# Kernel optimization log

Measured on AMD Instinct MI355X. Metric: run time of the kernel, lower is better.

The kernel has to match this reference:

```python
import jax, jax.numpy as jnp
import numpy as np

B, TV, TH, F, H, D = 16, 128, 64, 512, 512, 256


def setup_inputs() -> dict:
    key = jax.random.key(0)
    ks = jax.random.split(key, 6)
    return {
        "v": jax.random.normal(ks[0], (B, TV, F), dtype=jnp.float32),
        "h": jax.random.normal(ks[1], (B, TH, H), dtype=jnp.float32),
        "W": jax.random.normal(ks[2], (F, D), dtype=jnp.float32) * 0.05,
        "U": jax.random.normal(ks[3], (H, D), dtype=jnp.float32) * 0.05,
        "b": jax.random.normal(ks[4], (D,), dtype=jnp.float32) * 0.05,
        "w": jax.random.normal(ks[5], (D, 1), dtype=jnp.float32) * 0.05,
    }


def reference(v, h, W, U, b, w):
    # v: [B, Tv, F] video features; h: [B, Th, H] decoder hidden states
    Wv = jnp.einsum("btf,fd->btd", v, W)      # [B, Tv, D]
    Uh = jnp.einsum("bsh,hd->bsd", h, U)      # [B, Th, D]
    # Broadcast add -> [B, Th, Tv, D], tanh nonlinearity (additive attention)
    f = jnp.tanh(Uh[:, :, None, :] + Wv[:, None, :, :] + b)
    q = jnp.einsum("bstd,d->bst", f, w[:, 0])  # scores [B, Th, Tv]
    beta = jax.nn.softmax(q, axis=-1)           # softmax over Tv (axis -2 of q[..., None])
    u = jnp.einsum("bst,btf->bsf", beta, v)    # context [B, Th, F]
    return u
```

## Files before the change

kernel.cpp:

```cpp
#include <hip/hip_runtime.h>
#include <hip/hip_bf16.h>

#define BB 16
#define TV 128
#define TH 64
#define FF 512
#define HH 512
#define DD 256

#define LOG2E2 2.8853900817779268f

typedef __attribute__((ext_vector_type(8))) short bf16x8;
typedef __attribute__((ext_vector_type(4))) float f32x4;

__device__ __forceinline__ float fast_exp2(float x) {
#if __has_builtin(__builtin_amdgcn_exp2f)
  return __builtin_amdgcn_exp2f(x);
#else
  return __expf(x * 0.6931471805599453f);
#endif
}
__device__ __forceinline__ float fast_rcp(float x) {
#if __has_builtin(__builtin_amdgcn_rcpf)
  return __builtin_amdgcn_rcpf(x);
#else
  return 1.0f / x;
#endif
}
__device__ __forceinline__ unsigned short f2bf(float x) {
  union { float f; unsigned u; } a; a.f = x;
  unsigned r = a.u + 0x7fffu + ((a.u >> 16) & 1u);
  return (unsigned short)(r >> 16);
}
__device__ __forceinline__ float bf2f(unsigned short x) {
  union { unsigned u; float f; } a; a.u = ((unsigned)x) << 16;
  return a.f;
}

#define NT_V 262144
#define NT_H 131072
#define NT_W 32768
__global__ __launch_bounds__(256) void convert_kernel(
    const float* __restrict__ v, const float* __restrict__ h,
    const float* __restrict__ W, const float* __restrict__ U,
    unsigned short* __restrict__ vb, unsigned short* __restrict__ hb,
    unsigned short* __restrict__ WT, unsigned short* __restrict__ UT) {
  int task = blockIdx.x * 256 + threadIdx.x;
  if (task < NT_V) {
    float4 x = ((const float4*)v)[task];
    ushort4 o = make_ushort4(f2bf(x.x), f2bf(x.y), f2bf(x.z), f2bf(x.w));
    *(ushort4*)&vb[(size_t)task * 4] = o;
  } else if (task < NT_V + NT_H) {
    int t2 = task - NT_V;
    float4 x = ((const float4*)h)[t2];
    ushort4 o = make_ushort4(f2bf(x.x), f2bf(x.y), f2bf(x.z), f2bf(x.w));
    *(ushort4*)&hb[(size_t)t2 * 4] = o;
  } else {
    int t2 = task - NT_V - NT_H;
    const float* S;
    unsigned short* Dt;
    if (t2 < NT_W) { S = W; Dt = WT; } else { S = U; Dt = UT; t2 -= NT_W; }
    int n = t2 & 255, k4 = t2 >> 8;
    float a0 = S[(k4 * 4 + 0) * 256 + n];
    float a1 = S[(k4 * 4 + 1) * 256 + n];
    float a2 = S[(k4 * 4 + 2) * 256 + n];
    float a3 = S[(k4 * 4 + 3) * 256 + n];
    ushort4 o = make_ushort4(f2bf(a0), f2bf(a1), f2bf(a2), f2bf(a3));
    *(ushort4*)&Dt[(size_t)n * 512 + k4 * 4] = o;
  }
}

__global__ __launch_bounds__(256) void mfma_gemm_kernel(
    const unsigned short* __restrict__ Av, const unsigned short* __restrict__ Ah,
    const unsigned short* __restrict__ WT, const unsigned short* __restrict__ UT,
    const float* __restrict__ bias, float* __restrict__ Wv2T,
    float* __restrict__ Uh2) {
  const int bid = blockIdx.x;
  const unsigned short* A;
  const unsigned short* BT;
  int mt, nt;
  bool is_wv;
  if (bid < 128) {
    A = Av; BT = WT; is_wv = true;
    mt = bid >> 3; nt = bid & 7;
  } else {
    const int b2 = bid - 128;
    A = Ah; BT = UT; is_wv = false;
    mt = b2 >> 3; nt = b2 & 7;
  }
  const int wv   = threadIdx.x >> 6;
  const int lane = threadIdx.x & 63;
  const int m0   = mt * 128 + wv * 32;
  const int n0   = nt * 32;
  const int r16  = lane & 15;
  const int quad = lane >> 4;

  const unsigned short* a0p = A + (size_t)(m0 + r16) * 512 + quad * 8;
  const unsigned short* a1p = a0p + 16 * 512;
  const unsigned short* b0p = BT + (size_t)(n0 + r16) * 512 + quad * 8;
  const unsigned short* b1p = b0p + 16 * 512;

  f32x4 acc00 = {0.f, 0.f, 0.f, 0.f};
  f32x4 acc01 = {0.f, 0.f, 0.f, 0.f};
  f32x4 acc10 = {0.f, 0.f, 0.f, 0.f};
  f32x4 acc11 = {0.f, 0.f, 0.f, 0.f};

#pragma unroll 4
  for (int kc = 0; kc < 16; kc++) {
    bf16x8 a0 = *(const bf16x8*)(a0p + kc * 32);
    bf16x8 a1 = *(const bf16x8*)(a1p + kc * 32);
    bf16x8 b0 = *(const bf16x8*)(b0p + kc * 32);
    bf16x8 b1 = *(const bf16x8*)(b1p + kc * 32);
    acc00 = __builtin_amdgcn_mfma_f32_16x16x32_bf16(a0, b0, acc00, 0, 0, 0);
    acc01 = __builtin_amdgcn_mfma_f32_16x16x32_bf16(a0, b1, acc01, 0, 0, 0);
    acc10 = __builtin_amdgcn_mfma_f32_16x16x32_bf16(a1, b0, acc10, 0, 0, 0);
    acc11 = __builtin_amdgcn_mfma_f32_16x16x32_bf16(a1, b1, acc11, 0, 0, 0);
  }

  if (is_wv) {
    const int tb = (m0 & 127) + quad * 4;
    float* Wb = Wv2T + (size_t)mt * 32768;
    float4 s00, s01, s10, s11;
#pragma unroll
    for (int r = 0; r < 4; r++) {
      (&s00.x)[r] = acc00[r] * LOG2E2;
      (&s01.x)[r] = acc01[r] * LOG2E2;
      (&s10.x)[r] = acc10[r] * LOG2E2;
      (&s11.x)[r] = acc11[r] * LOG2E2;
    }
    *(float4*)&Wb[(size_t)(n0 + r16) * 128 + tb]           = s00;
    *(float4*)&Wb[(size_t)(n0 + r16) * 128 + tb + 16]      = s10;
    *(float4*)&Wb[(size_t)(n0 + 16 + r16) * 128 + tb]      = s01;
    *(float4*)&Wb[(size_t)(n0 + 16 + r16) * 128 + tb + 16] = s11;
  } else {
    const float bj0 = bias[n0 + r16];
    const float bj1 = bias[n0 + 16 + r16];
#pragma unroll
    for (int r = 0; r < 4; r++) {
      const int row0 = m0 + quad * 4 + r;
      Uh2[(size_t)row0 * 256 + n0 + r16]             = (acc00[r] + bj0) * LOG2E2;
      Uh2[(size_t)row0 * 256 + n0 + 16 + r16]        = (acc01[r] + bj1) * LOG2E2;
      Uh2[(size_t)(row0 + 16) * 256 + n0 + r16]      = (acc10[r] + bj0) * LOG2E2;
      Uh2[(size_t)(row0 + 16) * 256 + n0 + 16 + r16] = (acc11[r] + bj1) * LOG2E2;
    }
  }
}

__global__ __launch_bounds__(512) void attn_fused_kernel(
    const float* __restrict__ Wv2T, const float* __restrict__ Uh2,
    const float* __restrict__ wg, const unsigned short* __restrict__ vb16,
    float* __restrict__ u) {
  __shared__ float UhS[2 * 256];
  __shared__ float wS[256];
  __shared__ float pS[8 * 2 * 128];
  __shared__ float bS[2 * 128];
  __shared__ float mW[4];
  __shared__ float sW[4];

  const int tid = threadIdx.x;
  const int b   = blockIdx.x >> 5;
  const int sg  = blockIdx.x & 31;
  const int s0  = sg * 2;

  if (tid < 128) {
    const int row = tid >> 6, q4 = (tid & 63) << 2;
    *(float4*)&UhS[row * 256 + q4] =
        *(const float4*)&Uh2[(size_t)(b * 64 + s0 + row) * 256 + q4];
  } else if (tid < 192) {
    const int q4 = (tid - 128) << 2;
    *(float4*)&wS[q4] = *(const float4*)&wg[q4];
  }
  __syncthreads();

  {
    const int t4 = tid & 31;
    const int dg = (tid >> 5) & 7;
    const int s  = tid >> 8;
    const float* wvb = Wv2T + (size_t)b * 32768 + (size_t)dg * 32 * 128 + t4 * 4;
    const float4* uhq = (const float4*)&UhS[s * 256 + dg * 32];
    const float4* wq  = (const float4*)&wS[dg * 32];
    float4 acc = {0.f, 0.f, 0.f, 0.f};
#pragma unroll
    for (int jq = 0; jq < 8; jq++) {
      float4 uh4 = uhq[jq];
      float4 w4  = wq[jq];
#pragma unroll
      for (int jj = 0; jj < 4; jj++) {
        float4 a  = *(const float4*)(wvb + (jq * 4 + jj) * 128);
        float uh = (&uh4.x)[jj];
        float ww = (&w4.x)[jj];
        acc.x = fmaf(ww, fast_rcp(fast_exp2(a.x + uh) + 1.0f), acc.x);
        acc.y = fmaf(ww, fast_rcp(fast_exp2(a.y + uh) + 1.0f), acc.y);
        acc.z = fmaf(ww, fast_rcp(fast_exp2(a.z + uh) + 1.0f), acc.z);
        acc.w = fmaf(ww, fast_rcp(fast_exp2(a.w + uh) + 1.0f), acc.w);
      }
    }
    *(float4*)&pS[(dg * 2 + s) * 128 + t4 * 4] = acc;
  }
  __syncthreads();

  float qv = 0.0f, ev = 0.0f;
  const int wvid = tid >> 6, lane = tid & 63;
  if (tid < 256) {
    const int s_l = tid >> 7, t = tid & 127;
    float ssum = 0.0f;
#pragma unroll
    for (int dg = 0; dg < 8; dg++) ssum += pS[(dg * 2 + s_l) * 128 + t];
    qv = ssum * (-LOG2E2);
    float m = qv;
#pragma unroll
    for (int off = 32; off > 0; off >>= 1) m = fmaxf(m, __shfl_xor(m, off, 64));
    if (lane == 0) mW[wvid] = m;
  }
  __syncthreads();
  if (tid < 256) {
    float m = fmaxf(mW[wvid], mW[wvid ^ 1]);
    ev = fast_exp2(qv - m);
    float ssum = ev;
#pragma unroll
    for (int off = 32; off > 0; off >>= 1) ssum += __shfl_xor(ssum, off, 64);
    if (lane == 0) sW[wvid] = ssum;
  }
  __syncthreads();
  if (tid < 256) {
    const int s_l = tid >> 7, t = tid & 127;
    bS[s_l * 128 + t] = ev * fast_rcp(sW[wvid] + sW[wvid ^ 1]);
  }
  __syncthreads();

  const unsigned short* vb2 = vb16 + (size_t)b * TV * FF;
  const int f = tid;
  float a0 = 0.f, a1 = 0.f;
#pragma unroll 4
  for (int tg = 0; tg < 128; tg += 4) {
    float4 b0 = *(const float4*)&bS[0 * 128 + tg];
    float4 b1 = *(const float4*)&bS[1 * 128 + tg];
    float v0 = bf2f(vb2[(tg + 0) * 512 + f]);
    float v1 = bf2f(vb2[(tg + 1) * 512 + f]);
    float v2 = bf2f(vb2[(tg + 2) * 512 + f]);
    float v3 = bf2f(vb2[(tg + 3) * 512 + f]);
    a0 = fmaf(b0.x, v0, a0); a0 = fmaf(b0.y, v1, a0);
    a0 = fmaf(b0.z, v2, a0); a0 = fmaf(b0.w, v3, a0);
    a1 = fmaf(b1.x, v0, a1); a1 = fmaf(b1.y, v1, a1);
    a1 = fmaf(b1.z, v2, a1); a1 = fmaf(b1.w, v3, a1);
  }
  float* urow = u + (size_t)(b * 64 + s0) * 512;
  urow[0 * 512 + f] = a0;
  urow[1 * 512 + f] = a1;
}

extern "C" void kernel_launch(void* const* d_in, const int* in_sizes, int n_in,
                              void* d_out, int out_size, void* d_ws, size_t ws_size,
                              hipStream_t stream) {
  const float* v  = (const float*)d_in[0];
  const float* h  = (const float*)d_in[1];
  const float* W  = (const float*)d_in[2];
  const float* U  = (const float*)d_in[3];
  const float* bb = (const float*)d_in[4];
  const float* w  = (const float*)d_in[5];
  float* u = (float*)d_out;

  float* Wv2T = (float*)d_ws;
  float* Uh2  = Wv2T + (size_t)2048 * 256;
  unsigned short* vb16 = (unsigned short*)(Uh2 + (size_t)1024 * 256);
  unsigned short* hb16 = vb16 + (size_t)2048 * 512;
  unsigned short* WT   = hb16 + (size_t)1024 * 512;
  unsigned short* UT   = WT + (size_t)256 * 512;

  convert_kernel<<<1792, 256, 0, stream>>>(v, h, W, U, vb16, hb16, WT, UT);
  mfma_gemm_kernel<<<192, 256, 0, stream>>>(vb16, hb16, WT, UT, bb, Wv2T, Uh2);
  attn_fused_kernel<<<512, 512, 0, stream>>>(Wv2T, Uh2, w, vb16, u);
}
```

Measured before the change: 97.97 us.

## Fuse bf16 conversion into GEMM, stage transposed weights in LDS, drop convert kernel

Removes the separate conversion kernel. The GEMM now loads fp32 activations directly and packs them to bf16 in registers. Each block transposes its W/U slice into padded LDS as bf16. The attention context pass reads fp32 v directly instead of the bf16 copy. This saves one launch and the extra write/read round trip through the workspace. In exchange, each GEMM block redundantly converts its weight slice, and the A loads and the final v reads move twice as many bytes.

New measurement: 98.93 us. About the same (+1.0%).

```diff
diff --git a/kernel.cpp b/kernel.cpp
--- a/kernel.cpp
+++ b/kernel.cpp
@@ -32,73 +32,63 @@
   unsigned r = a.u + 0x7fffu + ((a.u >> 16) & 1u);
   return (unsigned short)(r >> 16);
 }
-__device__ __forceinline__ float bf2f(unsigned short x) {
-  union { unsigned u; float f; } a; a.u = ((unsigned)x) << 16;
-  return a.f;
-}
-
-#define NT_V 262144
-#define NT_H 131072
-#define NT_W 32768
-__global__ __launch_bounds__(256) void convert_kernel(
+__device__ __forceinline__ bf16x8 pack_bf8(float4 lo, float4 hi) {
+  bf16x8 r;
+  r[0] = (short)f2bf(lo.x); r[1] = (short)f2bf(lo.y);
+  r[2] = (short)f2bf(lo.z); r[3] = (short)f2bf(lo.w);
+  r[4] = (short)f2bf(hi.x); r[5] = (short)f2bf(hi.y);
+  r[6] = (short)f2bf(hi.z); r[7] = (short)f2bf(hi.w);
+  return r;
+}
+
+#define BT_STRIDE 520
+__global__ __launch_bounds__(256) void mfma_gemm_kernel(
     const float* __restrict__ v, const float* __restrict__ h,
     const float* __restrict__ W, const float* __restrict__ U,
-    unsigned short* __restrict__ vb, unsigned short* __restrict__ hb,
-    unsigned short* __restrict__ WT, unsigned short* __restrict__ UT) {
-  int task = blockIdx.x * 256 + threadIdx.x;
-  if (task < NT_V) {
-    float4 x = ((const float4*)v)[task];
-    ushort4 o = make_ushort4(f2bf(x.x), f2bf(x.y), f2bf(x.z), f2bf(x.w));
-    *(ushort4*)&vb[(size_t)task * 4] = o;
-  } else if (task < NT_V + NT_H) {
-    int t2 = task - NT_V;
-    float4 x = ((const float4*)h)[t2];
-    ushort4 o = make_ushort4(f2bf(x.x), f2bf(x.y), f2bf(x.z), f2bf(x.w));
-    *(ushort4*)&hb[(size_t)t2 * 4] = o;
-  } else {
-    int t2 = task - NT_V - NT_H;
-    const float* S;
-    unsigned short* Dt;
-    if (t2 < NT_W) { S = W; Dt = WT; } else { S = U; Dt = UT; t2 -= NT_W; }
-    int n = t2 & 255, k4 = t2 >> 8;
-    float a0 = S[(k4 * 4 + 0) * 256 + n];
-    float a1 = S[(k4 * 4 + 1) * 256 + n];
-    float a2 = S[(k4 * 4 + 2) * 256 + n];
-    float a3 = S[(k4 * 4 + 3) * 256 + n];
-    ushort4 o = make_ushort4(f2bf(a0), f2bf(a1), f2bf(a2), f2bf(a3));
-    *(ushort4*)&Dt[(size_t)n * 512 + k4 * 4] = o;
-  }
-}
-
-__global__ __launch_bounds__(256) void mfma_gemm_kernel(
-    const unsigned short* __restrict__ Av, const unsigned short* __restrict__ Ah,
-    const unsigned short* __restrict__ WT, const unsigned short* __restrict__ UT,
     const float* __restrict__ bias, float* __restrict__ Wv2T,
     float* __restrict__ Uh2) {
+  __shared__ unsigned short BTs[32 * BT_STRIDE];
+
   const int bid = blockIdx.x;
-  const unsigned short* A;
-  const unsigned short* BT;
+  const float* A;
+  const float* Bsrc;
   int mt, nt;
   bool is_wv;
   if (bid < 128) {
-    A = Av; BT = WT; is_wv = true;
+    A = v; Bsrc = W; is_wv = true;
     mt = bid >> 3; nt = bid & 7;
   } else {
     const int b2 = bid - 128;
-    A = Ah; BT = UT; is_wv = false;
+    A = h; Bsrc = U; is_wv = false;
     mt = b2 >> 3; nt = b2 & 7;
   }
-  const int wv   = threadIdx.x >> 6;
-  const int lane = threadIdx.x & 63;
+  const int tid  = threadIdx.x;
+  const int wv   = tid >> 6;
+  const int lane = tid & 63;
   const int m0   = mt * 128 + wv * 32;
   const int n0   = nt * 32;
   const int r16  = lane & 15;
   const int quad = lane >> 4;
 
-  const unsigned short* a0p = A + (size_t)(m0 + r16) * 512 + quad * 8;
-  const unsigned short* a1p = a0p + 16 * 512;
-  const unsigned short* b0p = BT + (size_t)(n0 + r16) * 512 + quad * 8;
-  const unsigned short* b1p = b0p + 16 * 512;
+  {
+    const int kr = tid >> 3;
+    const int c4 = (tid & 7) << 2;
+#pragma unroll 4
+    for (int p = 0; p < 16; p++) {
+      const int k = p * 32 + kr;
+      float4 wrow = *(const float4*)&Bsrc[(size_t)k * 256 + n0 + c4];
+      BTs[(c4 + 0) * BT_STRIDE + k] = f2bf(wrow.x);
+      BTs[(c4 + 1) * BT_STRIDE + k] = f2bf(wrow.y);
+      BTs[(c4 + 2) * BT_STRIDE + k] = f2bf(wrow.z);
+      BTs[(c4 + 3) * BT_STRIDE + k] = f2bf(wrow.w);
+    }
+  }
+  __syncthreads();
+
+  const float* a0p = A + (size_t)(m0 + r16) * 512 + quad * 8;
+  const float* a1p = a0p + 16 * 512;
+  const unsigned short* bt0 = &BTs[r16 * BT_STRIDE + quad * 8];
+  const unsigned short* bt1 = &BTs[(16 + r16) * BT_STRIDE + quad * 8];
 
   f32x4 acc00 = {0.f, 0.f, 0.f, 0.f};
   f32x4 acc01 = {0.f, 0.f, 0.f, 0.f};
@@ -107,10 +97,14 @@
 
 #pragma unroll 4
   for (int kc = 0; kc < 16; kc++) {
-    bf16x8 a0 = *(const bf16x8*)(a0p + kc * 32);
-    bf16x8 a1 = *(const bf16x8*)(a1p + kc * 32);
-    bf16x8 b0 = *(const bf16x8*)(b0p + kc * 32);
-    bf16x8 b1 = *(const bf16x8*)(b1p + kc * 32);
+    float4 a0lo = *(const float4*)(a0p + kc * 32);
+    float4 a0hi = *(const float4*)(a0p + kc * 32 + 4);
+    float4 a1lo = *(const float4*)(a1p + kc * 32);
+    float4 a1hi = *(const float4*)(a1p + kc * 32 + 4);
+    bf16x8 a0 = pack_bf8(a0lo, a0hi);
+    bf16x8 a1 = pack_bf8(a1lo, a1hi);
+    bf16x8 b0 = *(const bf16x8*)(bt0 + kc * 32);
+    bf16x8 b1 = *(const bf16x8*)(bt1 + kc * 32);
     acc00 = __builtin_amdgcn_mfma_f32_16x16x32_bf16(a0, b0, acc00, 0, 0, 0);
     acc01 = __builtin_amdgcn_mfma_f32_16x16x32_bf16(a0, b1, acc01, 0, 0, 0);
     acc10 = __builtin_amdgcn_mfma_f32_16x16x32_bf16(a1, b0, acc10, 0, 0, 0);
@@ -148,7 +142,7 @@
 
 __global__ __launch_bounds__(512) void attn_fused_kernel(
     const float* __restrict__ Wv2T, const float* __restrict__ Uh2,
-    const float* __restrict__ wg, const unsigned short* __restrict__ vb16,
+    const float* __restrict__ wg, const float* __restrict__ v,
     float* __restrict__ u) {
   __shared__ float UhS[2 * 256];
   __shared__ float wS[256];
@@ -228,17 +222,17 @@
   }
   __syncthreads();
 
-  const unsigned short* vb2 = vb16 + (size_t)b * TV * FF;
+  const float* vb2 = v + (size_t)b * TV * FF;
   const int f = tid;
   float a0 = 0.f, a1 = 0.f;
 #pragma unroll 4
   for (int tg = 0; tg < 128; tg += 4) {
     float4 b0 = *(const float4*)&bS[0 * 128 + tg];
     float4 b1 = *(const float4*)&bS[1 * 128 + tg];
-    float v0 = bf2f(vb2[(tg + 0) * 512 + f]);
-    float v1 = bf2f(vb2[(tg + 1) * 512 + f]);
-    float v2 = bf2f(vb2[(tg + 2) * 512 + f]);
-    float v3 = bf2f(vb2[(tg + 3) * 512 + f]);
+    float v0 = vb2[(tg + 0) * 512 + f];
+    float v1 = vb2[(tg + 1) * 512 + f];
+    float v2 = vb2[(tg + 2) * 512 + f];
+    float v3 = vb2[(tg + 3) * 512 + f];
     a0 = fmaf(b0.x, v0, a0); a0 = fmaf(b0.y, v1, a0);
     a0 = fmaf(b0.z, v2, a0); a0 = fmaf(b0.w, v3, a0);
     a1 = fmaf(b1.x, v0, a1); a1 = fmaf(b1.y, v1, a1);
@@ -262,12 +256,7 @@
 
   float* Wv2T = (float*)d_ws;
   float* Uh2  = Wv2T + (size_t)2048 * 256;
-  unsigned short* vb16 = (unsigned short*)(Uh2 + (size_t)1024 * 256);
-  unsigned short* hb16 = vb16 + (size_t)2048 * 512;
-  unsigned short* WT   = hb16 + (size_t)1024 * 512;
-  unsigned short* UT   = WT + (size_t)256 * 512;
-
-  convert_kernel<<<1792, 256, 0, stream>>>(v, h, W, U, vb16, hb16, WT, UT);
-  mfma_gemm_kernel<<<192, 256, 0, stream>>>(vb16, hb16, WT, UT, bb, Wv2T, Uh2);
-  attn_fused_kernel<<<512, 512, 0, stream>>>(Wv2T, Uh2, w, vb16, u);
-}
+
+  mfma_gemm_kernel<<<192, 256, 0, stream>>>(v, h, W, U, bb, Wv2T, Uh2);
+  attn_fused_kernel<<<512, 512, 0, stream>>>(Wv2T, Uh2, w, v, u);
+}
```
